# Performance work log

Measured on AMD Instinct MI355X. Metric: run time of the kernel, lower is better.

Reference implementation:

```python
import jax, jax.numpy as jnp
import numpy as np

N_NODES = 100000
N_EDGES = 1600000
N_GRAPHS = 2000
F_IN = 16
HEADS = 8
C = 16            # per-head out channels (hidden_dim)
HC = HEADS * C    # 128
N_CLASSES = 2
NEG_SLOPE = 0.2   # PyG GATConv default leaky_relu slope


def setup_inputs() -> dict:
    key = jax.random.key(0)
    ks = jax.random.split(key, 12)
    x = jax.random.normal(ks[0], (N_NODES, F_IN), dtype=jnp.float32)
    edge_index = jax.random.randint(ks[1], (2, N_EDGES), 0, N_NODES, dtype=jnp.int32)
    batch = jnp.sort(jax.random.randint(ks[2], (N_NODES,), 0, N_GRAPHS, dtype=jnp.int32))
    s1 = 1.0 / np.sqrt(F_IN)
    s2 = 1.0 / np.sqrt(HC)
    return {
        "x": x,
        "edge_index": edge_index,
        "batch": batch,
        "W1": jax.random.normal(ks[3], (F_IN, HC), dtype=jnp.float32) * s1,
        "a1_src": jax.random.normal(ks[4], (HEADS, C), dtype=jnp.float32) * s2,
        "a1_dst": jax.random.normal(ks[5], (HEADS, C), dtype=jnp.float32) * s2,
        "b1": jnp.zeros((HC,), dtype=jnp.float32),
        "W2": jax.random.normal(ks[6], (HC, HC), dtype=jnp.float32) * s2,
        "a2_src": jax.random.normal(ks[7], (HEADS, C), dtype=jnp.float32) * s2,
        "a2_dst": jax.random.normal(ks[8], (HEADS, C), dtype=jnp.float32) * s2,
        "b2": jnp.zeros((HC,), dtype=jnp.float32),
        "lin_W": jax.random.normal(ks[9], (HC, N_CLASSES), dtype=jnp.float32) * s2,
        "lin_b": jnp.zeros((N_CLASSES,), dtype=jnp.float32),
    }


def gat_layer(h_in, src, dst, W, a_src, a_dst, b, num_nodes):
    # h: [N, H, C] per-head transformed features
    h = (h_in @ W).reshape(num_nodes, HEADS, C)
    # per-node attention half-logits: [N, H]
    logit_src = jnp.einsum('nhc,hc->nh', h, a_src)
    logit_dst = jnp.einsum('nhc,hc->nh', h, a_dst)
    # per-edge logits [E, H]
    e = jax.nn.leaky_relu(logit_src[src] + logit_dst[dst], NEG_SLOPE)
    # segment softmax over incoming edges of each destination node
    m = jax.ops.segment_max(e, dst, num_segments=num_nodes)
    m = jnp.where(jnp.isfinite(m), m, 0.0)
    ex = jnp.exp(e - m[dst])
    denom = jax.ops.segment_sum(ex, dst, num_segments=num_nodes)
    alpha = ex / jnp.maximum(denom[dst], 1e-16)
    # weighted scatter-add aggregation: [N, H, C]
    out = jax.ops.segment_sum(alpha[:, :, None] * h[src], dst, num_segments=num_nodes)
    return out.reshape(num_nodes, HC) + b


def reference(x, edge_index, batch, W1, a1_src, a1_dst, b1, W2, a2_src, a2_dst, b2, lin_W, lin_b):
    n = x.shape[0]
    # PyG GATConv adds self-loops by default
    loops = jnp.arange(n, dtype=edge_index.dtype)
    src = jnp.concatenate([edge_index[0], loops])
    dst = jnp.concatenate([edge_index[1], loops])
    h = jax.nn.relu(gat_layer(x, src, dst, W1, a1_src, a1_dst, b1, n))
    h = jax.nn.relu(gat_layer(h, src, dst, W2, a2_src, a2_dst, b2, n))
    # global mean pool per graph
    sums = jax.ops.segment_sum(h, batch, num_segments=N_GRAPHS)
    counts = jax.ops.segment_sum(jnp.ones((n, 1), h.dtype), batch, num_segments=N_GRAPHS)
    pooled = sums / jnp.maximum(counts, 1.0)
    logits = pooled @ lin_W + lin_b
    return jax.nn.softmax(logits, axis=1)
```

## Files before the change

kernel.cpp:

```cpp
#include <hip/hip_runtime.h>
#include <math.h>

#define N_NODES 100000
#define N_EDGESI 1600000
#define E_TOTAL (N_EDGESI + N_NODES)
#define N_GRAPHS 2000
#define F_IN 16
#define HEADS 8
#define CPH 16
#define HC 128
#define NEG 0.2f

#define BSHIFT 9
#define BNODES (1<<BSHIFT)
#define NBUK ((N_NODES + BNODES - 1)/BNODES)
#define BCAP 12288
#define BIN_EPT 16
#define BIN_TPB 256
#define BIN_EPB (BIN_EPT*BIN_TPB)
#define NBIN_BLK ((E_TOTAL + BIN_EPB - 1)/BIN_EPB)

#define GOFF_BLK ((N_NODES+255)/256)
#define WCONV_BLK ((HC*HC)/256)

typedef __bf16 bf16x8 __attribute__((ext_vector_type(8)));
typedef float  f32x4  __attribute__((ext_vector_type(4)));

__device__ __forceinline__ float leaky(float x){ return fmaxf(x, NEG*x); }
__device__ __forceinline__ float bf2f(unsigned short u){ return __uint_as_float(((unsigned)u)<<16); }
__device__ __forceinline__ unsigned short f2bf(float f){
  unsigned u = __float_as_uint(f);
  unsigned r = (u + 0x7fffu + ((u>>16)&1u)) >> 16;
  return (unsigned short)r;
}
__device__ __forceinline__ float blo(unsigned u){ return __uint_as_float(u<<16); }
__device__ __forceinline__ float bhi(unsigned u){ return __uint_as_float(u & 0xffff0000u); }

__global__ void k_bin(const int* __restrict__ ei, int* __restrict__ gpos, unsigned* __restrict__ gbin){
  __shared__ unsigned bcnt[NBUK];
  __shared__ unsigned bbase[NBUK];
  int t = threadIdx.x;
  for (int i = t; i < NBUK; i += BIN_TPB) bcnt[i] = 0;
  __syncthreads();
  int base = blockIdx.x*BIN_EPB;
  unsigned entry[BIN_EPT]; unsigned meta[BIN_EPT];
  #pragma unroll
  for (int i = 0; i < BIN_EPT; ++i){
    int e = base + i*BIN_TPB + t;
    if (e < E_TOTAL){
      unsigned s, d;
      if (e < N_EDGESI){ s = (unsigned)ei[e]; d = (unsigned)ei[N_EDGESI + e]; }
      else { s = d = (unsigned)(e - N_EDGESI); }
      unsigned b = d >> BSHIFT;
      unsigned r = atomicAdd(&bcnt[b], 1u);
      entry[i] = ((d & (BNODES-1u)) << 17) | s;
      meta[i] = (r << 8) | b;
    } else meta[i] = 0xffffffffu;
  }
  __syncthreads();
  for (int i = t; i < NBUK; i += BIN_TPB) bbase[i] = (unsigned)atomicAdd(&gpos[i], (int)bcnt[i]);
  __syncthreads();
  #pragma unroll
  for (int i = 0; i < BIN_EPT; ++i){
    if (meta[i] != 0xffffffffu){
      unsigned b = meta[i] & 0xffu;
      unsigned r = meta[i] >> 8;
      gbin[(size_t)b*BCAP + bbase[b] + r] = entry[i];
    }
  }
}

__global__ void k_misc(const int* __restrict__ batch, int* __restrict__ goff,
                       const float* __restrict__ W, unsigned short* __restrict__ Wt,
                       const int* __restrict__ gpos, int* __restrict__ gbase){
  int blk = blockIdx.x;
  if (blk < GOFF_BLK){
    int n = blk*256 + threadIdx.x;
    if (n >= N_NODES) return;
    int b = batch[n];
    if (n == 0){ for (int g = 0; g <= b; ++g) goff[g] = 0; }
    int b1 = (n+1 < N_NODES) ? batch[n+1] : N_GRAPHS;
    for (int g = b+1; g <= b1; ++g) goff[g] = n+1;
  } else if (blk < GOFF_BLK + WCONV_BLK){
    int i = (blk - GOFF_BLK)*256 + threadIdx.x;
    if (i >= HC*HC) return;
    int c = i >> 7, k = i & 127;
    Wt[i] = f2bf(W[k*HC + c]);
  } else {
    __shared__ int ws[4];
    int t = threadIdx.x, lane = t & 63, wv = t >> 6;
    int v = (t < NBUK) ? gpos[t] : 0;
    int sc = v;
    #pragma unroll
    for (int o=1;o<64;o<<=1){ int u = __shfl_up(sc,o,64); if (lane>=o) sc += u; }
    if (lane==63) ws[wv] = sc;
    __syncthreads();
    if (wv==0 && lane<4){
      int w2 = ws[lane];
      #pragma unroll
      for (int o=1;o<4;o<<=1){ int u = __shfl_up(w2,o,64); if (lane>=o) w2 += u; }
      ws[lane] = w2;
    }
    __syncthreads();
    int base = wv ? ws[wv-1] : 0;
    if (t < NBUK) gbase[t] = base + sc - v;
  }
}

__global__ __launch_bounds__(512) void k_csr(const int* __restrict__ gpos, const int* __restrict__ gbase,
                      const unsigned* __restrict__ gbin,
                      int* __restrict__ off, int* __restrict__ csrc){
  __shared__ unsigned ent[BCAP];
  __shared__ int lcnt[BNODES];
  __shared__ int wsum[8];
  int b = blockIdx.x, t = threadIdx.x;
  int nb = __builtin_amdgcn_readfirstlane(gpos[b]);
  int base = __builtin_amdgcn_readfirstlane(gbase[b]);
  const unsigned* bb = gbin + (size_t)b*BCAP;
  for (int i = t; i < nb; i += 512) ent[i] = bb[i];
  lcnt[t] = 0;
  __syncthreads();
  for (int i = t; i < nb; i += 512) atomicAdd(&lcnt[ent[i] >> 17], 1);
  __syncthreads();
  int lane = t & 63, wv = t >> 6;
  int v = lcnt[t];
  int sc = v;
  #pragma unroll
  for (int o = 1; o < 64; o <<= 1){ int u = __shfl_up(sc, o, 64); if (lane >= o) sc += u; }
  if (lane == 63) wsum[wv] = sc;
  __syncthreads();
  if (wv == 0 && lane < 8){
    int w2 = wsum[lane];
    #pragma unroll
    for (int o = 1; o < 8; o <<= 1){ int u = __shfl_up(w2, o, 64); if (lane >= o) w2 += u; }
    wsum[lane] = w2;
  }
  __syncthreads();
  int excl = (wv ? wsum[wv-1] : 0) + sc - v;
  int d = (b << BSHIFT) + t;
  if (d < N_NODES) off[d] = base + excl;
  if (b == NBUK-1 && t == 0) off[N_NODES] = E_TOTAL;
  __syncthreads();
  lcnt[t] = base + excl;
  __syncthreads();
  for (int i = t; i < nb; i += 512){
    unsigned en = ent[i];
    int p = atomicAdd(&lcnt[en >> 17], 1);
    csrc[p] = (int)(en & 0x1ffffu);
  }
}

__global__ void k_gemm1(const float* __restrict__ x, const float* __restrict__ W,
                        const float* __restrict__ asrc, const float* __restrict__ adst,
                        unsigned short* __restrict__ hb,
                        float* __restrict__ ls, float* __restrict__ ld){
  int i = blockIdx.x*256 + threadIdx.x;
  if (i >= N_NODES*64) return;
  int n = i >> 6, cp = i & 63;
  const float* xr = x + n*F_IN;
  const float2* W2v = (const float2*)W;
  float a0 = 0.f, a1 = 0.f;
  #pragma unroll
  for (int k = 0; k < F_IN; ++k){
    float xv = xr[k];
    float2 w = W2v[k*64 + cp];
    a0 += xv*w.x; a1 += xv*w.y;
  }
  ushort2 o; o.x = f2bf(a0); o.y = f2bf(a1);
  ((ushort2*)hb)[i] = o;
  int h = cp >> 3;
  int cih = 2*(cp & 7);
  float2 asv = *(const float2*)(asrc + h*CPH + cih);
  float2 adv = *(const float2*)(adst + h*CPH + cih);
  float ps = a0*asv.x + a1*asv.y;
  float pd = a0*adv.x + a1*adv.y;
  #pragma unroll
  for (int o2 = 1; o2 < 8; o2 <<= 1){ ps += __shfl_xor(ps, o2, 64); pd += __shfl_xor(pd, o2, 64); }
  if ((cp & 7) == 0){
    ls[n*8 + h] = ps;
    ld[n*8 + h] = pd;
  }
}

__global__ void k_gemm2_mfma(const unsigned short* __restrict__ hin,
                             const unsigned short* __restrict__ w2t,
                             const float* __restrict__ asrc, const float* __restrict__ adst,
                             unsigned short* __restrict__ hb,
                             float* __restrict__ ls, float* __restrict__ ld){
  int t = threadIdx.x, lane = t & 63, wv = t >> 6;
  int n0 = blockIdx.x*64 + wv*16;
  int rowl = lane & 15, kgrp = lane >> 4;
  int row = n0 + rowl;
  int rowc = (row < N_NODES) ? row : (N_NODES-1);
  bf16x8 a[4];
  #pragma unroll
  for (int ks = 0; ks < 4; ++ks)
    a[ks] = *(const bf16x8*)(hin + (size_t)rowc*HC + ks*32 + kgrp*8);
  #pragma unroll
  for (int ct = 0; ct < 8; ++ct){
    f32x4 acc = {0.f, 0.f, 0.f, 0.f};
    int col = ct*16 + rowl;
    #pragma unroll
    for (int ks = 0; ks < 4; ++ks){
      bf16x8 b = *(const bf16x8*)(w2t + (size_t)col*HC + ks*32 + kgrp*8);
      acc = __builtin_amdgcn_mfma_f32_16x16x32_bf16(a[ks], b, acc, 0, 0, 0);
    }
    float asv = asrc[ct*CPH + rowl];
    float adv = adst[ct*CPH + rowl];
    #pragma unroll
    for (int r = 0; r < 4; ++r){
      int ro = n0 + kgrp*4 + r;
      if (ro < N_NODES) hb[(size_t)ro*HC + col] = f2bf(acc[r]);
      float pls = acc[r]*asv, pld = acc[r]*adv;
      #pragma unroll
      for (int o = 1; o < 16; o <<= 1){ pls += __shfl_xor(pls, o, 64); pld += __shfl_xor(pld, o, 64); }
      if (rowl == 0 && ro < N_NODES){
        ls[ro*8 + ct] = pls;
        ld[ro*8 + ct] = pld;
      }
    }
  }
}

__global__ void k_agg(const int* __restrict__ off, const int* __restrict__ csrc,
                      const unsigned short* __restrict__ hb, const float* __restrict__ ls,
                      const float* __restrict__ ld, const float* __restrict__ bias,
                      unsigned short* __restrict__ outb){
  int wid = threadIdx.x >> 6, lane = threadIdx.x & 63;
  int n = blockIdx.x*4 + wid;
  if (n >= N_NODES) return;
  int rs = __builtin_amdgcn_readfirstlane(off[n]);
  int re = __builtin_amdgcn_readfirstlane(off[n+1]);
  int q = lane >> 4;
  int l = lane & 15;
  int h = l >> 1;
  float ldh = ld[n*8 + h];
  const uint4* hb4 = (const uint4*)hb;
  float ac0=0.f, ac1=0.f, ac2=0.f, ac3=0.f, ac4=0.f, ac5=0.f, ac6=0.f, ac7=0.f, dsum=0.f;
  #define AGG_BODY(EE) { \
    int s = csrc[EE]; \
    float g = ls[s*8 + h]; \
    float ex = __expf(leaky(g + ldh)); \
    uint4 v = hb4[(size_t)s*16 + l]; \
    ac0 += ex*blo(v.x); ac1 += ex*bhi(v.x); \
    ac2 += ex*blo(v.y); ac3 += ex*bhi(v.y); \
    ac4 += ex*blo(v.z); ac5 += ex*bhi(v.z); \
    ac6 += ex*blo(v.w); ac7 += ex*bhi(v.w); \
    dsum += ex; }
  int base = rs;
  for (; base + 16 <= re; base += 16){
    AGG_BODY(base+q); AGG_BODY(base+q+4); AGG_BODY(base+q+8); AGG_BODY(base+q+12);
  }
  for (int ee = base + q; ee < re; ee += 4) AGG_BODY(ee);
  #undef AGG_BODY
  ac0 += __shfl_xor(ac0,16,64); ac0 += __shfl_xor(ac0,32,64);
  ac1 += __shfl_xor(ac1,16,64); ac1 += __shfl_xor(ac1,32,64);
  ac2 += __shfl_xor(ac2,16,64); ac2 += __shfl_xor(ac2,32,64);
  ac3 += __shfl_xor(ac3,16,64); ac3 += __shfl_xor(ac3,32,64);
  ac4 += __shfl_xor(ac4,16,64); ac4 += __shfl_xor(ac4,32,64);
  ac5 += __shfl_xor(ac5,16,64); ac5 += __shfl_xor(ac5,32,64);
  ac6 += __shfl_xor(ac6,16,64); ac6 += __shfl_xor(ac6,32,64);
  ac7 += __shfl_xor(ac7,16,64); ac7 += __shfl_xor(ac7,32,64);
  dsum += __shfl_xor(dsum,16,64); dsum += __shfl_xor(dsum,32,64);
  if (q == 0){
    float inv = 1.f/fmaxf(dsum, 1e-16f);
    float4 b0 = ((const float4*)bias)[l*2];
    float4 b1 = ((const float4*)bias)[l*2+1];
    uint4 o;
    o.x = (unsigned)f2bf(fmaxf(ac0*inv + b0.x, 0.f)) | ((unsigned)f2bf(fmaxf(ac1*inv + b0.y, 0.f)) << 16);
    o.y = (unsigned)f2bf(fmaxf(ac2*inv + b0.z, 0.f)) | ((unsigned)f2bf(fmaxf(ac3*inv + b0.w, 0.f)) << 16);
    o.z = (unsigned)f2bf(fmaxf(ac4*inv + b1.x, 0.f)) | ((unsigned)f2bf(fmaxf(ac5*inv + b1.y, 0.f)) << 16);
    o.w = (unsigned)f2bf(fmaxf(ac6*inv + b1.z, 0.f)) | ((unsigned)f2bf(fmaxf(ac7*inv + b1.w, 0.f)) << 16);
    ((uint4*)outb)[(size_t)n*16 + l] = o;
  }
}

__global__ void k_poolcls(const unsigned short* __restrict__ h, const int* __restrict__ goff,
                          const float* __restrict__ lw, const float* __restrict__ lb,
                          float* __restrict__ out){
  __shared__ float sh[4][HC];
  int g = blockIdx.x;
  int t = threadIdx.x, lane = t & 63, wv = t >> 6;
  int s = goff[g], epos = goff[g+1];
  float a0 = 0.f, a1 = 0.f;
  const ushort2* h2 = (const ushort2*)h;
  for (int n = s + wv; n < epos; n += 4){
    ushort2 v = h2[(size_t)n*64 + lane];
    a0 += bf2f(v.x); a1 += bf2f(v.y);
  }
  sh[wv][lane*2] = a0; sh[wv][lane*2+1] = a1;
  __syncthreads();
  if (wv == 0){
    int c0 = lane*2;
    float p0 = sh[0][c0] + sh[1][c0] + sh[2][c0] + sh[3][c0];
    float p1 = sh[0][c0+1] + sh[1][c0+1] + sh[2][c0+1] + sh[3][c0+1];
    int cntg = epos - s;
    float invc = 1.f/fmaxf((float)cntg, 1.f);
    float v0 = p0*invc, v1 = p1*invc;
    float l0 = v0*lw[c0*2+0] + v1*lw[(c0+1)*2+0];
    float l1 = v0*lw[c0*2+1] + v1*lw[(c0+1)*2+1];
    #pragma unroll
    for (int o = 32; o >= 1; o >>= 1){ l0 += __shfl_xor(l0,o,64); l1 += __shfl_xor(l1,o,64); }
    if (lane == 0){
      l0 += lb[0]; l1 += lb[1];
      float m = fmaxf(l0,l1);
      float e0 = __expf(l0-m), e1 = __expf(l1-m);
      float si = e0 + e1;
      out[g*2]   = e0/si;
      out[g*2+1] = e1/si;
    }
  }
}

extern "C" void kernel_launch(void* const* d_in, const int* in_sizes, int n_in,
                              void* d_out, int out_size, void* d_ws, size_t ws_size,
                              hipStream_t stream){
  const float* x   = (const float*)d_in[0];
  const int*   ei  = (const int*)d_in[1];
  const int*   bat = (const int*)d_in[2];
  const float* W1  = (const float*)d_in[3];
  const float* a1s = (const float*)d_in[4];
  const float* a1d = (const float*)d_in[5];
  const float* b1  = (const float*)d_in[6];
  const float* W2  = (const float*)d_in[7];
  const float* a2s = (const float*)d_in[8];
  const float* a2d = (const float*)d_in[9];
  const float* b2  = (const float*)d_in[10];
  const float* lw  = (const float*)d_in[11];
  const float* lb  = (const float*)d_in[12];
  float* out = (float*)d_out;

  char* w = (char*)d_ws;
  auto alloc = [&](size_t bytes)->void*{ void* p = (void*)w; w += (bytes + 511) & ~size_t(511); return p; };
  int* off    = (int*)alloc((size_t)(N_NODES+1)*4);
  int* csrc   = (int*)alloc((size_t)E_TOTAL*4);
  int* goff   = (int*)alloc((size_t)(N_GRAPHS+1)*4);
  int* gpos   = (int*)alloc((size_t)NBUK*4);
  int* gbase  = (int*)alloc((size_t)NBUK*4);
  unsigned* gbin = (unsigned*)alloc((size_t)NBUK*BCAP*4);
  unsigned short* w2t  = (unsigned short*)alloc((size_t)HC*HC*2);
  unsigned short* hbf  = (unsigned short*)alloc((size_t)N_NODES*HC*2);
  unsigned short* hbf2 = (unsigned short*)alloc((size_t)N_NODES*HC*2);
  float* lsb  = (float*)alloc((size_t)N_NODES*HEADS*4);
  float* ldb  = (float*)alloc((size_t)N_NODES*HEADS*4);

  hipMemsetAsync(gpos, 0, (size_t)NBUK*4, stream);

  k_bin  <<<NBIN_BLK,BIN_TPB,0,stream>>>(ei, gpos, gbin);
  k_misc <<<GOFF_BLK + WCONV_BLK + 1,256,0,stream>>>(bat, goff, W2, w2t, gpos, gbase);
  k_csr  <<<NBUK,512,0,stream>>>(gpos, gbase, gbin, off, csrc);

  k_gemm1 <<<(N_NODES*64)/256,256,0,stream>>>(x, W1, a1s, a1d, hbf, lsb, ldb);
  k_agg   <<<(N_NODES+3)/4,256,0,stream>>>(off, csrc, hbf, lsb, ldb, b1, hbf2);
  k_gemm2_mfma<<<(N_NODES+63)/64,256,0,stream>>>(hbf2, w2t, a2s, a2d, hbf, lsb, ldb);
  k_agg   <<<(N_NODES+3)/4,256,0,stream>>>(off, csrc, hbf, lsb, ldb, b2, hbf2);

  k_poolcls<<<N_GRAPHS,256,0,stream>>>(hbf2, goff, lw, lb, out);
}
```

Baseline: 321.2 us.

## Merge preprocessing kernels, locally sort bins, and overlap gemm1 with CSR build

Binning, batch-offset and weight-conversion work now run in one launch. The bin kernel sorts its edges by bucket in shared memory first, so the global writes to each bucket are contiguous instead of scattered. The separate scan kernel is removed: each CSR block recomputes its bucket base with a serial prefix sum over bucket counts. The layer-1 feature transform runs as extra blocks of the CSR launch so the two can overlap. This cuts launch count and scatter cost, but adds a serial loop per CSR block and more shared memory in the bin blocks.

```diff
diff --git a/kernel.cpp b/kernel.cpp
--- a/kernel.cpp
+++ b/kernel.cpp
@@ -22,6 +22,7 @@
 
 #define GOFF_BLK ((N_NODES+255)/256)
 #define WCONV_BLK ((HC*HC)/256)
+#define GEMM1_BLK ((N_NODES*64 + 511)/512)
 
 typedef __bf16 bf16x8 __attribute__((ext_vector_type(8)));
 typedef float  f32x4  __attribute__((ext_vector_type(4)));
@@ -36,149 +37,166 @@
 __device__ __forceinline__ float blo(unsigned u){ return __uint_as_float(u<<16); }
 __device__ __forceinline__ float bhi(unsigned u){ return __uint_as_float(u & 0xffff0000u); }
 
-__global__ void k_bin(const int* __restrict__ ei, int* __restrict__ gpos, unsigned* __restrict__ gbin){
-  __shared__ unsigned bcnt[NBUK];
-  __shared__ unsigned bbase[NBUK];
-  int t = threadIdx.x;
-  for (int i = t; i < NBUK; i += BIN_TPB) bcnt[i] = 0;
-  __syncthreads();
-  int base = blockIdx.x*BIN_EPB;
-  unsigned entry[BIN_EPT]; unsigned meta[BIN_EPT];
-  #pragma unroll
-  for (int i = 0; i < BIN_EPT; ++i){
-    int e = base + i*BIN_TPB + t;
-    if (e < E_TOTAL){
-      unsigned s, d;
-      if (e < N_EDGESI){ s = (unsigned)ei[e]; d = (unsigned)ei[N_EDGESI + e]; }
-      else { s = d = (unsigned)(e - N_EDGESI); }
-      unsigned b = d >> BSHIFT;
-      unsigned r = atomicAdd(&bcnt[b], 1u);
-      entry[i] = ((d & (BNODES-1u)) << 17) | s;
-      meta[i] = (r << 8) | b;
-    } else meta[i] = 0xffffffffu;
-  }
-  __syncthreads();
-  for (int i = t; i < NBUK; i += BIN_TPB) bbase[i] = (unsigned)atomicAdd(&gpos[i], (int)bcnt[i]);
-  __syncthreads();
-  #pragma unroll
-  for (int i = 0; i < BIN_EPT; ++i){
-    if (meta[i] != 0xffffffffu){
-      unsigned b = meta[i] & 0xffu;
-      unsigned r = meta[i] >> 8;
-      gbin[(size_t)b*BCAP + bbase[b] + r] = entry[i];
-    }
-  }
-}
-
-__global__ void k_misc(const int* __restrict__ batch, int* __restrict__ goff,
-                       const float* __restrict__ W, unsigned short* __restrict__ Wt,
-                       const int* __restrict__ gpos, int* __restrict__ gbase){
+__global__ void k_pre(const int* __restrict__ ei, int* __restrict__ gpos, unsigned* __restrict__ gbin,
+                      const int* __restrict__ batch, int* __restrict__ goff,
+                      const float* __restrict__ W, unsigned short* __restrict__ Wt){
   int blk = blockIdx.x;
-  if (blk < GOFF_BLK){
-    int n = blk*256 + threadIdx.x;
+  if (blk < NBIN_BLK){
+    __shared__ int cnt[NBUK];
+    __shared__ int lofs[NBUK];
+    __shared__ int bbase[NBUK];
+    __shared__ int ws[4];
+    __shared__ unsigned sorted[BIN_EPB];
+    __shared__ unsigned short sbkt[BIN_EPB];
+    int t = threadIdx.x;
+    for (int i = t; i < NBUK; i += BIN_TPB) cnt[i] = 0;
+    __syncthreads();
+    int base = blk*BIN_EPB;
+    unsigned entry[BIN_EPT]; int ebkt[BIN_EPT]; int erank[BIN_EPT];
+    #pragma unroll
+    for (int i = 0; i < BIN_EPT; ++i){
+      int e = base + i*BIN_TPB + t;
+      if (e < E_TOTAL){
+        unsigned s, d;
+        if (e < N_EDGESI){ s = (unsigned)ei[e]; d = (unsigned)ei[N_EDGESI + e]; }
+        else { s = d = (unsigned)(e - N_EDGESI); }
+        int b = (int)(d >> BSHIFT);
+        erank[i] = atomicAdd(&cnt[b], 1);
+        ebkt[i] = b;
+        entry[i] = ((d & (BNODES-1u)) << 17) | s;
+      } else ebkt[i] = -1;
+    }
+    __syncthreads();
+    {
+      int lane = t & 63, wv = t >> 6;
+      int v = (t < NBUK) ? cnt[t] : 0;
+      int sc = v;
+      #pragma unroll
+      for (int o = 1; o < 64; o <<= 1){ int u = __shfl_up(sc, o, 64); if (lane >= o) sc += u; }
+      if (lane == 63) ws[wv] = sc;
+      __syncthreads();
+      if (wv == 0 && lane < 4){
+        int w2 = ws[lane];
+        #pragma unroll
+        for (int o = 1; o < 4; o <<= 1){ int u = __shfl_up(w2, o, 64); if (lane >= o) w2 += u; }
+        ws[lane] = w2;
+      }
+      __syncthreads();
+      if (t < NBUK){
+        lofs[t] = (wv ? ws[wv-1] : 0) + sc - v;
+        bbase[t] = v ? atomicAdd(&gpos[t], v) : 0;
+      }
+    }
+    __syncthreads();
+    #pragma unroll
+    for (int i = 0; i < BIN_EPT; ++i){
+      if (ebkt[i] >= 0){
+        int p = lofs[ebkt[i]] + erank[i];
+        sorted[p] = entry[i];
+        sbkt[p] = (unsigned short)ebkt[i];
+      }
+    }
+    __syncthreads();
+    int nval = E_TOTAL - base; if (nval > BIN_EPB) nval = BIN_EPB;
+    for (int i = t; i < nval; i += BIN_TPB){
+      int b = sbkt[i];
+      gbin[(size_t)b*BCAP + bbase[b] + (i - lofs[b])] = sorted[i];
+    }
+  } else if (blk < NBIN_BLK + GOFF_BLK){
+    int n = (blk - NBIN_BLK)*256 + threadIdx.x;
     if (n >= N_NODES) return;
     int b = batch[n];
     if (n == 0){ for (int g = 0; g <= b; ++g) goff[g] = 0; }
     int b1 = (n+1 < N_NODES) ? batch[n+1] : N_GRAPHS;
     for (int g = b+1; g <= b1; ++g) goff[g] = n+1;
-  } else if (blk < GOFF_BLK + WCONV_BLK){
-    int i = (blk - GOFF_BLK)*256 + threadIdx.x;
+  } else {
+    int i = (blk - NBIN_BLK - GOFF_BLK)*256 + threadIdx.x;
     if (i >= HC*HC) return;
     int c = i >> 7, k = i & 127;
     Wt[i] = f2bf(W[k*HC + c]);
-  } else {
-    __shared__ int ws[4];
-    int t = threadIdx.x, lane = t & 63, wv = t >> 6;
-    int v = (t < NBUK) ? gpos[t] : 0;
-    int sc = v;
-    #pragma unroll
-    for (int o=1;o<64;o<<=1){ int u = __shfl_up(sc,o,64); if (lane>=o) sc += u; }
-    if (lane==63) ws[wv] = sc;
-    __syncthreads();
-    if (wv==0 && lane<4){
-      int w2 = ws[lane];
-      #pragma unroll
-      for (int o=1;o<4;o<<=1){ int u = __shfl_up(w2,o,64); if (lane>=o) w2 += u; }
-      ws[lane] = w2;
-    }
-    __syncthreads();
-    int base = wv ? ws[wv-1] : 0;
-    if (t < NBUK) gbase[t] = base + sc - v;
-  }
-}
-
-__global__ __launch_bounds__(512) void k_csr(const int* __restrict__ gpos, const int* __restrict__ gbase,
-                      const unsigned* __restrict__ gbin,
-                      int* __restrict__ off, int* __restrict__ csrc){
+  }
+}
+
+__global__ __launch_bounds__(512) void k_csr2(
+                      const int* __restrict__ gpos, const unsigned* __restrict__ gbin,
+                      int* __restrict__ off, int* __restrict__ csrc,
+                      const float* __restrict__ x, const float* __restrict__ W1,
+                      const float* __restrict__ asrc, const float* __restrict__ adst,
+                      unsigned short* __restrict__ hb,
+                      float* __restrict__ ls, float* __restrict__ ld){
   __shared__ unsigned ent[BCAP];
   __shared__ int lcnt[BNODES];
   __shared__ int wsum[8];
-  int b = blockIdx.x, t = threadIdx.x;
-  int nb = __builtin_amdgcn_readfirstlane(gpos[b]);
-  int base = __builtin_amdgcn_readfirstlane(gbase[b]);
-  const unsigned* bb = gbin + (size_t)b*BCAP;
-  for (int i = t; i < nb; i += 512) ent[i] = bb[i];
-  lcnt[t] = 0;
-  __syncthreads();
-  for (int i = t; i < nb; i += 512) atomicAdd(&lcnt[ent[i] >> 17], 1);
-  __syncthreads();
-  int lane = t & 63, wv = t >> 6;
-  int v = lcnt[t];
-  int sc = v;
-  #pragma unroll
-  for (int o = 1; o < 64; o <<= 1){ int u = __shfl_up(sc, o, 64); if (lane >= o) sc += u; }
-  if (lane == 63) wsum[wv] = sc;
-  __syncthreads();
-  if (wv == 0 && lane < 8){
-    int w2 = wsum[lane];
-    #pragma unroll
-    for (int o = 1; o < 8; o <<= 1){ int u = __shfl_up(w2, o, 64); if (lane >= o) w2 += u; }
-    wsum[lane] = w2;
-  }
-  __syncthreads();
-  int excl = (wv ? wsum[wv-1] : 0) + sc - v;
-  int d = (b << BSHIFT) + t;
-  if (d < N_NODES) off[d] = base + excl;
-  if (b == NBUK-1 && t == 0) off[N_NODES] = E_TOTAL;
-  __syncthreads();
-  lcnt[t] = base + excl;
-  __syncthreads();
-  for (int i = t; i < nb; i += 512){
-    unsigned en = ent[i];
-    int p = atomicAdd(&lcnt[en >> 17], 1);
-    csrc[p] = (int)(en & 0x1ffffu);
-  }
-}
-
-__global__ void k_gemm1(const float* __restrict__ x, const float* __restrict__ W,
-                        const float* __restrict__ asrc, const float* __restrict__ adst,
-                        unsigned short* __restrict__ hb,
-                        float* __restrict__ ls, float* __restrict__ ld){
-  int i = blockIdx.x*256 + threadIdx.x;
-  if (i >= N_NODES*64) return;
-  int n = i >> 6, cp = i & 63;
-  const float* xr = x + n*F_IN;
-  const float2* W2v = (const float2*)W;
-  float a0 = 0.f, a1 = 0.f;
-  #pragma unroll
-  for (int k = 0; k < F_IN; ++k){
-    float xv = xr[k];
-    float2 w = W2v[k*64 + cp];
-    a0 += xv*w.x; a1 += xv*w.y;
-  }
-  ushort2 o; o.x = f2bf(a0); o.y = f2bf(a1);
-  ((ushort2*)hb)[i] = o;
-  int h = cp >> 3;
-  int cih = 2*(cp & 7);
-  float2 asv = *(const float2*)(asrc + h*CPH + cih);
-  float2 adv = *(const float2*)(adst + h*CPH + cih);
-  float ps = a0*asv.x + a1*asv.y;
-  float pd = a0*adv.x + a1*adv.y;
-  #pragma unroll
-  for (int o2 = 1; o2 < 8; o2 <<= 1){ ps += __shfl_xor(ps, o2, 64); pd += __shfl_xor(pd, o2, 64); }
-  if ((cp & 7) == 0){
-    ls[n*8 + h] = ps;
-    ld[n*8 + h] = pd;
+  __shared__ int gp[NBUK];
+  __shared__ int sbase;
+  int blk = blockIdx.x;
+  if (blk < NBUK){
+    int b = blk, t = threadIdx.x;
+    for (int i = t; i < NBUK; i += 512) gp[i] = gpos[i];
+    lcnt[t] = 0;
+    __syncthreads();
+    if (t == 0){ int s = 0; for (int j = 0; j < b; ++j) s += gp[j]; sbase = s; }
+    int nb = gp[b];
+    const unsigned* bb = gbin + (size_t)b*BCAP;
+    for (int i = t; i < nb; i += 512) ent[i] = bb[i];
+    __syncthreads();
+    int base = sbase;
+    for (int i = t; i < nb; i += 512) atomicAdd(&lcnt[ent[i] >> 17], 1);
+    __syncthreads();
+    int lane = t & 63, wv = t >> 6;
+    int v = lcnt[t];
+    int sc = v;
+    #pragma unroll
+    for (int o = 1; o < 64; o <<= 1){ int u = __shfl_up(sc, o, 64); if (lane >= o) sc += u; }
+    if (lane == 63) wsum[wv] = sc;
+    __syncthreads();
+    if (wv == 0 && lane < 8){
+      int w2 = wsum[lane];
+      #pragma unroll
+      for (int o = 1; o < 8; o <<= 1){ int u = __shfl_up(w2, o, 64); if (lane >= o) w2 += u; }
+      wsum[lane] = w2;
+    }
+    __syncthreads();
+    int excl = (wv ? wsum[wv-1] : 0) + sc - v;
+    int d = (b << BSHIFT) + t;
+    if (d < N_NODES) off[d] = base + excl;
+    if (b == NBUK-1 && t == 0) off[N_NODES] = E_TOTAL;
+    __syncthreads();
+    lcnt[t] = base + excl;
+    __syncthreads();
+    for (int i = t; i < nb; i += 512){
+      unsigned en = ent[i];
+      int p = atomicAdd(&lcnt[en >> 17], 1);
+      csrc[p] = (int)(en & 0x1ffffu);
+    }
+  } else {
+    int i = (blk - NBUK)*512 + threadIdx.x;
+    if (i >= N_NODES*64) return;
+    int n = i >> 6, cp = i & 63;
+    const float* xr = x + n*F_IN;
+    const float2* W2v = (const float2*)W1;
+    float a0 = 0.f, a1 = 0.f;
+    #pragma unroll
+    for (int k = 0; k < F_IN; ++k){
+      float xv = xr[k];
+      float w = 0.f;  (void)w;
+      float2 wv2 = W2v[k*64 + cp];
+      a0 += xv*wv2.x; a1 += xv*wv2.y;
+    }
+    ushort2 o; o.x = f2bf(a0); o.y = f2bf(a1);
+    ((ushort2*)hb)[i] = o;
+    int h = cp >> 3;
+    int cih = 2*(cp & 7);
+    float2 asv = *(const float2*)(asrc + h*CPH + cih);
+    float2 adv = *(const float2*)(adst + h*CPH + cih);
+    float ps = a0*asv.x + a1*asv.y;
+    float pd = a0*adv.x + a1*adv.y;
+    #pragma unroll
+    for (int o2 = 1; o2 < 8; o2 <<= 1){ ps += __shfl_xor(ps, o2, 64); pd += __shfl_xor(pd, o2, 64); }
+    if ((cp & 7) == 0){
+      ls[n*8 + h] = ps;
+      ld[n*8 + h] = pd;
+    }
   }
 }
 
@@ -336,7 +354,6 @@
   int* csrc   = (int*)alloc((size_t)E_TOTAL*4);
   int* goff   = (int*)alloc((size_t)(N_GRAPHS+1)*4);
   int* gpos   = (int*)alloc((size_t)NBUK*4);
-  int* gbase  = (int*)alloc((size_t)NBUK*4);
   unsigned* gbin = (unsigned*)alloc((size_t)NBUK*BCAP*4);
   unsigned short* w2t  = (unsigned short*)alloc((size_t)HC*HC*2);
   unsigned short* hbf  = (unsigned short*)alloc((size_t)N_NODES*HC*2);
@@ -346,14 +363,12 @@
 
   hipMemsetAsync(gpos, 0, (size_t)NBUK*4, stream);
 
-  k_bin  <<<NBIN_BLK,BIN_TPB,0,stream>>>(ei, gpos, gbin);
-  k_misc <<<GOFF_BLK + WCONV_BLK + 1,256,0,stream>>>(bat, goff, W2, w2t, gpos, gbase);
-  k_csr  <<<NBUK,512,0,stream>>>(gpos, gbase, gbin, off, csrc);
-
-  k_gemm1 <<<(N_NODES*64)/256,256,0,stream>>>(x, W1, a1s, a1d, hbf, lsb, ldb);
-  k_agg   <<<(N_NODES+3)/4,256,0,stream>>>(off, csrc, hbf, lsb, ldb, b1, hbf2);
+  k_pre  <<<NBIN_BLK + GOFF_BLK + WCONV_BLK,BIN_TPB,0,stream>>>(ei, gpos, gbin, bat, goff, W2, w2t);
+  k_csr2 <<<NBUK + GEMM1_BLK,512,0,stream>>>(gpos, gbin, off, csrc, x, W1, a1s, a1d, hbf, lsb, ldb);
+
+  k_agg  <<<(N_NODES+3)/4,256,0,stream>>>(off, csrc, hbf, lsb, ldb, b1, hbf2);
   k_gemm2_mfma<<<(N_NODES+63)/64,256,0,stream>>>(hbf2, w2t, a2s, a2d, hbf, lsb, ldb);
-  k_agg   <<<(N_NODES+3)/4,256,0,stream>>>(off, csrc, hbf, lsb, ldb, b2, hbf2);
+  k_agg  <<<(N_NODES+3)/4,256,0,stream>>>(off, csrc, hbf, lsb, ldb, b2, hbf2);
 
   k_poolcls<<<N_GRAPHS,256,0,stream>>>(hbf2, goff, lw, lb, out);
 }
```

Measured after the change: 309.1 us. 3.7% less time.
